# Optimization experiments

Measured on AMD Instinct MI355X. Metric: run time of the kernel, lower is better.

The kernel has to match this reference:

```python
import jax, jax.numpy as jnp
import numpy as np

BETA = 0.1
MARGIN = 0.1
LOSS_WEIGHT = 1.0
K = 4          # num_negative_samples_per_positive
EPS = 1e-6
C, D, P = 100000, 256, 65536


def _energy(p, c):
    """Euclidean entailment-cone energy: relu(apex_angle(p,c) - aperture(p))."""
    diff = c - p
    num = jnp.sum(c * c, -1) - jnp.sum(p * p, -1) - jnp.sum(diff * diff, -1)
    norm_p = jnp.linalg.norm(p, axis=-1)
    denom = 2.0 * norm_p * jnp.linalg.norm(diff, axis=-1) + EPS
    cosang = jnp.clip(num / denom, -1.0 + EPS, 1.0 - EPS)
    ang = jnp.arccos(cosang)
    aperture = jnp.arcsin(jnp.clip(BETA / (norm_p + EPS), 0.0, 1.0 - EPS))
    return jax.nn.relu(ang - aperture)


def setup_inputs() -> dict:
    key = jax.random.key(0)
    k1, k2, k3 = jax.random.split(key, 3)
    prototypes = jax.random.normal(k1, (C, D), dtype=jnp.float32)
    pairs = jax.random.randint(k2, (P, 2), 0, C, dtype=jnp.int32)
    neg_c = jax.random.randint(k3, (P * K,), 0, C, dtype=jnp.int32)
    return {"prototypes": prototypes, "pairs": pairs, "neg_c": neg_c}


def reference(prototypes, pairs, neg_c):
    # positive pairs: (parent, child) gathers
    p_pos = prototypes[pairs[:, 0]]                    # [P, D]
    c_pos = prototypes[pairs[:, 1]]                    # [P, D]
    avg_pos = _energy(p_pos, c_pos).mean()

    # negatives: each positive parent repeated K times vs sampled neg children
    neg_p_idx = jnp.repeat(pairs[:, 0], K)             # [P*K]
    p_neg = prototypes[neg_p_idx]                      # [P*K, D]
    c_neg = prototypes[neg_c]                          # [P*K, D]
    avg_neg = jax.nn.relu(MARGIN - _energy(p_neg, c_neg)).mean()

    return (avg_pos + avg_neg) * 0.5 * LOSS_WEIGHT
```

## Files before the change

kernel.cpp:

```cpp
#include <hip/hip_runtime.h>

#define BETA   0.1f
#define MARGIN 0.1f
#define EPSF   1e-6f
#define KNEG   4

__device__ __forceinline__ float gsum16(float v) {
    #pragma unroll
    for (int off = 8; off >= 1; off >>= 1) v += __shfl_xor(v, off, 64);
    return v;
}
__device__ __forceinline__ float gmax16(float v) {
    #pragma unroll
    for (int off = 8; off >= 1; off >>= 1) v = fmaxf(v, __shfl_xor(v, off, 64));
    return v;
}
__device__ __forceinline__ float wave_sum(float v) {
    #pragma unroll
    for (int off = 32; off >= 1; off >>= 1) v += __shfl_xor(v, off, 64);
    return v;
}
__device__ __forceinline__ float dot4(float4 a, float4 b) {
    return a.x*b.x + a.y*b.y + a.z*b.z + a.w*b.w;
}

__global__ __launch_bounds__(256) void cvt_i4(
    const float* __restrict__ in, uint2* __restrict__ tab,
    float4* __restrict__ side, int C)
{
    const int sl  = threadIdx.x & 15;
    const int row = (blockIdx.x * 256 + threadIdx.x) >> 4;
    if (row >= C) return;
    const float4* src = (const float4*)(in + (size_t)row * 256);
    float4 v0 = src[4*sl+0], v1 = src[4*sl+1], v2 = src[4*sl+2], v3 = src[4*sl+3];
    float f[16] = { v0.x, v0.y, v0.z, v0.w,  v1.x, v1.y, v1.z, v1.w,
                    v2.x, v2.y, v2.z, v2.w,  v3.x, v3.y, v3.z, v3.w };
    float am = 0.f;
    #pragma unroll
    for (int d = 0; d < 16; ++d) am = fmaxf(am, fabsf(f[d]));
    am = gmax16(am);
    const float inv = (am > 0.f) ? (7.5f / am) : 0.f;
    unsigned u0 = 0, u1 = 0;
    #pragma unroll
    for (int n = 0; n < 8; ++n) {
        int c = (int)rintf(f[n] * inv);
        c = (c < -8) ? -8 : ((c > 7) ? 7 : c);
        u0 |= (unsigned)(c + 8) << (4 * n);
    }
    #pragma unroll
    for (int n = 0; n < 8; ++n) {
        int c = (int)rintf(f[8 + n] * inv);
        c = (c < -8) ? -8 : ((c > 7) ? 7 : c);
        u1 |= (unsigned)(c + 8) << (4 * n);
    }
    tab[(size_t)row * 16 + sl] = make_uint2(u0, u1);
    float ss = gsum16(dot4(v0,v0) + dot4(v1,v1) + dot4(v2,v2) + dot4(v3,v3));
    if (sl == 0) {
        float np = sqrtf(ss);
        float ap = asinf(fminf(fmaxf(BETA / (np + EPSF), 0.f), 1.f - EPSF));
        side[row] = make_float4(ss, ap, am * (1.f / 7.5f), 0.f);
    }
}

__device__ __forceinline__ float codes_dot(uint2 cu, const float* pf) {
    float acc = 0.f;
    #pragma unroll
    for (int n = 0; n < 8; ++n)
        acc = fmaf((float)((cu.x >> (4*n)) & 0xF), pf[n], acc);
    #pragma unroll
    for (int n = 0; n < 8; ++n)
        acc = fmaf((float)((cu.y >> (4*n)) & 0xF), pf[8 + n], acc);
    return acc;
}

__global__ __launch_bounds__(256) void cone_main_i4(
    const uint2*  __restrict__ tab,
    const float4* __restrict__ side,
    const int*    __restrict__ pairs,
    const int*    __restrict__ negc,
    float*        __restrict__ part,
    int P)
{
    const int lane = threadIdx.x & 63;
    const int wid  = threadIdx.x >> 6;
    const int sub  = lane >> 4;
    const int sl   = lane & 15;
    const int pair = (blockIdx.x * 4 + wid) * 4 + sub;

    float pos_e = 0.f, neg_e = 0.f;
    if (pair < P) {
        const int pi = pairs[2 * pair];
        const int i0 = pairs[2 * pair + 1];
        const int i1 = negc[4 * pair + 0];
        const int i2 = negc[4 * pair + 1];
        const int i3 = negc[4 * pair + 2];
        const int i4 = negc[4 * pair + 3];

        uint2 pu  = tab[(size_t)pi * 16 + sl];
        uint2 cu0 = tab[(size_t)i0 * 16 + sl];
        uint2 cu1 = tab[(size_t)i1 * 16 + sl];
        uint2 cu2 = tab[(size_t)i2 * 16 + sl];
        uint2 cu3 = tab[(size_t)i3 * 16 + sl];
        uint2 cu4 = tab[(size_t)i4 * 16 + sl];

        int tidx = pi;
        tidx = (sl == 1) ? i0 : tidx;
        tidx = (sl == 2) ? i1 : tidx;
        tidx = (sl == 3) ? i2 : tidx;
        tidx = (sl == 4) ? i3 : tidx;
        tidx = (sl == 5) ? i4 : tidx;
        float4 sd = side[tidx];

        const int base = sub * 16;
        const float p2 = __shfl(sd.x, base + 0, 64);
        const float ap = __shfl(sd.y, base + 0, 64);
        const float sp = __shfl(sd.z, base + 0, 64);
        const float np = sqrtf(p2);

        float pf[16];
        #pragma unroll
        for (int n = 0; n < 8; ++n) pf[n]     = (float)((pu.x >> (4*n)) & 0xF) - 8.f;
        #pragma unroll
        for (int n = 0; n < 8; ++n) pf[8 + n] = (float)((pu.y >> (4*n)) & 0xF) - 8.f;
        float s = 0.f;
        #pragma unroll
        for (int d = 0; d < 16; ++d) s += pf[d];
        const float SP = gsum16(s);

#define CONE_STEP(J, CU)                                                      \
        {                                                                     \
            const float draw = gsum16(codes_dot(CU, pf)) - 8.f * SP;          \
            const float c2 = __shfl(sd.x, base + 1 + J, 64);                  \
            const float sc = __shfl(sd.z, base + 1 + J, 64);                  \
            const float dot = draw * sp * sc;                                 \
            const float num = 2.f * (dot - p2);                               \
            const float d2  = fmaxf(c2 + p2 - 2.f * dot, 0.f);                \
            const float den = 2.f * np * sqrtf(d2) + EPSF;                    \
            const float ca  = fminf(fmaxf(num / den, -1.f + EPSF), 1.f - EPSF);\
            const float e   = fmaxf(acosf(ca) - ap, 0.f);                     \
            if (J == 0) pos_e = e;                                            \
            else        neg_e += fmaxf(MARGIN - e, 0.f);                      \
        }
        CONE_STEP(0, cu0)
        CONE_STEP(1, cu1)
        CONE_STEP(2, cu2)
        CONE_STEP(3, cu3)
        CONE_STEP(4, cu4)
#undef CONE_STEP
    }

    __shared__ float spos[16], sneg[16];
    if (sl == 0) { spos[wid * 4 + sub] = pos_e; sneg[wid * 4 + sub] = neg_e; }
    __syncthreads();
    if (threadIdx.x == 0) {
        float ps = 0.f, ns = 0.f;
        #pragma unroll
        for (int i = 0; i < 16; ++i) { ps += spos[i]; ns += sneg[i]; }
        part[2 * blockIdx.x]     = ps;
        part[2 * blockIdx.x + 1] = ns;
    }
}

__global__ __launch_bounds__(256) void cone_main_f32(
    const float* __restrict__ proto,
    const int*   __restrict__ pairs,
    const int*   __restrict__ negc,
    float*       __restrict__ part,
    int P)
{
    const int lane = threadIdx.x & 63;
    const int wid  = threadIdx.x >> 6;
    const int sub  = lane >> 4;
    const int sl   = lane & 15;
    const int pair = (blockIdx.x * 4 + wid) * 4 + sub;

    float pos_e = 0.f, neg_e = 0.f;
    if (pair < P) {
        const int pi = pairs[2 * pair];
        const int i0 = pairs[2 * pair + 1];
        const int i1 = negc[4 * pair + 0];
        const int i2 = negc[4 * pair + 1];
        const int i3 = negc[4 * pair + 2];
        const int i4 = negc[4 * pair + 3];

        const float4* prow = (const float4*)(proto + (size_t)pi * 256);
        float4 pv[4];
        #pragma unroll
        for (int r = 0; r < 4; ++r) pv[r] = prow[sl + 16 * r];

        float pp = 0.f;
        #pragma unroll
        for (int r = 0; r < 4; ++r) pp += dot4(pv[r], pv[r]);
        float p2     = gsum16(pp);
        float norm_p = sqrtf(p2);
        float apert  = asinf(fminf(fmaxf(BETA / (norm_p + EPSF), 0.f), 1.f - EPSF));

#define CONE_F32_STEP(J, IDX)                                                 \
        {                                                                     \
            const float4* crow = (const float4*)(proto + (size_t)(IDX) * 256);\
            float cc = 0.f, dd = 0.f;                                         \
            _Pragma("unroll")                                                 \
            for (int r = 0; r < 4; ++r) {                                     \
                float4 c = crow[sl + 16 * r], p = pv[r];                      \
                cc += dot4(c, c);                                             \
                float dx = c.x-p.x, dy = c.y-p.y, dz = c.z-p.z, dw = c.w-p.w; \
                dd += dx*dx + dy*dy + dz*dz + dw*dw;                          \
            }                                                                 \
            float c2 = gsum16(cc);                                            \
            float d2 = gsum16(dd);                                            \
            float num    = c2 - p2 - d2;                                      \
            float den    = 2.f * norm_p * sqrtf(d2) + EPSF;                   \
            float cosang = fminf(fmaxf(num / den, -1.f + EPSF), 1.f - EPSF);  \
            float e      = fmaxf(acosf(cosang) - apert, 0.f);                 \
            if (J == 0) pos_e = e;                                            \
            else        neg_e += fmaxf(MARGIN - e, 0.f);                      \
        }
        CONE_F32_STEP(0, i0)
        CONE_F32_STEP(1, i1)
        CONE_F32_STEP(2, i2)
        CONE_F32_STEP(3, i3)
        CONE_F32_STEP(4, i4)
#undef CONE_F32_STEP
    }

    __shared__ float sp[16], sn[16];
    if (sl == 0) { sp[wid * 4 + sub] = pos_e; sn[wid * 4 + sub] = neg_e; }
    __syncthreads();
    if (threadIdx.x == 0) {
        float ps = 0.f, ns = 0.f;
        #pragma unroll
        for (int i = 0; i < 16; ++i) { ps += sp[i]; ns += sn[i]; }
        part[2 * blockIdx.x]     = ps;
        part[2 * blockIdx.x + 1] = ns;
    }
}

__global__ __launch_bounds__(1024) void cone_final(
    const float* __restrict__ part, float* __restrict__ out, int nblocks, int P)
{
    float ps = 0.f, ns = 0.f;
    for (int i = threadIdx.x; i < nblocks; i += 1024) {
        ps += part[2 * i];
        ns += part[2 * i + 1];
    }
    ps = wave_sum(ps);
    ns = wave_sum(ns);
    const int lane = threadIdx.x & 63, wid = threadIdx.x >> 6;
    __shared__ float sp[16], sn[16];
    if (lane == 0) { sp[wid] = ps; sn[wid] = ns; }
    __syncthreads();
    if (threadIdx.x == 0) {
        float tp = 0.f, tn = 0.f;
        #pragma unroll
        for (int i = 0; i < 16; ++i) { tp += sp[i]; tn += sn[i]; }
        float fP = (float)P;
        out[0] = (tp / fP + tn / (fP * (float)KNEG)) * 0.5f;
    }
}

extern "C" void kernel_launch(void* const* d_in, const int* in_sizes, int n_in,
                              void* d_out, int out_size, void* d_ws, size_t ws_size,
                              hipStream_t stream) {
    const float* proto = (const float*)d_in[0];
    const int*   pairs = (const int*)d_in[1];
    const int*   negc  = (const int*)d_in[2];
    const int P = in_sizes[1] / 2;
    const int C = in_sizes[0] / 256;
    const int nblocks = (P + 15) / 16;

    const size_t tab_bytes  = (size_t)C * 128;
    const size_t side_bytes = (size_t)C * 16;
    const size_t part_bytes = (size_t)nblocks * 2 * sizeof(float);
    const size_t need = tab_bytes + side_bytes + part_bytes;

    if (ws_size >= need) {
        char* base = (char*)d_ws;
        uint2*  tab  = (uint2*)base;
        float4* side = (float4*)(base + tab_bytes);
        float*  part = (float*)(base + tab_bytes + side_bytes);

        cvt_i4<<<(C + 15) / 16, 256, 0, stream>>>(proto, tab, side, C);
        cone_main_i4<<<nblocks, 256, 0, stream>>>(tab, side, pairs, negc, part, P);
        cone_final<<<1, 1024, 0, stream>>>(part, (float*)d_out, nblocks, P);
    } else {
        float* part = (float*)d_ws;
        cone_main_f32<<<nblocks, 256, 0, stream>>>(proto, pairs, negc, part, P);
        cone_final<<<1, 1024, 0, stream>>>(part, (float*)d_out, nblocks, P);
    }
}
```

Measured before the change: 172.3 us.

## Use signed int4 codes with sdot8 and spread acos across lanes

Quantization now stores signed 4-bit codes at scale 7 instead of offset codes at 7.5, so the per-row dot products can use the hardware sdot8 integer instruction with an integer group reduction. This replaces the float unpack-and-fma loop and the offset correction term. The five acos evaluations per pair are spread across lanes, each lane computing one, followed by a reduction. The coarser quantization scale slightly changes accuracy.

```diff
diff --git a/kernel.cpp b/kernel.cpp
--- a/kernel.cpp
+++ b/kernel.cpp
@@ -6,6 +6,11 @@
 #define KNEG   4
 
 __device__ __forceinline__ float gsum16(float v) {
+    #pragma unroll
+    for (int off = 8; off >= 1; off >>= 1) v += __shfl_xor(v, off, 64);
+    return v;
+}
+__device__ __forceinline__ int gsum16i(int v) {
     #pragma unroll
     for (int off = 8; off >= 1; off >>= 1) v += __shfl_xor(v, off, 64);
     return v;
@@ -39,38 +44,49 @@
     #pragma unroll
     for (int d = 0; d < 16; ++d) am = fmaxf(am, fabsf(f[d]));
     am = gmax16(am);
-    const float inv = (am > 0.f) ? (7.5f / am) : 0.f;
+    const float inv = (am > 0.f) ? (7.0f / am) : 0.f;
     unsigned u0 = 0, u1 = 0;
     #pragma unroll
     for (int n = 0; n < 8; ++n) {
         int c = (int)rintf(f[n] * inv);
         c = (c < -8) ? -8 : ((c > 7) ? 7 : c);
-        u0 |= (unsigned)(c + 8) << (4 * n);
+        u0 |= ((unsigned)c & 0xFu) << (4 * n);
     }
     #pragma unroll
     for (int n = 0; n < 8; ++n) {
         int c = (int)rintf(f[8 + n] * inv);
         c = (c < -8) ? -8 : ((c > 7) ? 7 : c);
-        u1 |= (unsigned)(c + 8) << (4 * n);
+        u1 |= ((unsigned)c & 0xFu) << (4 * n);
     }
     tab[(size_t)row * 16 + sl] = make_uint2(u0, u1);
     float ss = gsum16(dot4(v0,v0) + dot4(v1,v1) + dot4(v2,v2) + dot4(v3,v3));
     if (sl == 0) {
         float np = sqrtf(ss);
         float ap = asinf(fminf(fmaxf(BETA / (np + EPSF), 0.f), 1.f - EPSF));
-        side[row] = make_float4(ss, ap, am * (1.f / 7.5f), 0.f);
-    }
-}
-
-__device__ __forceinline__ float codes_dot(uint2 cu, const float* pf) {
-    float acc = 0.f;
-    #pragma unroll
-    for (int n = 0; n < 8; ++n)
-        acc = fmaf((float)((cu.x >> (4*n)) & 0xF), pf[n], acc);
-    #pragma unroll
-    for (int n = 0; n < 8; ++n)
-        acc = fmaf((float)((cu.y >> (4*n)) & 0xF), pf[8 + n], acc);
+        side[row] = make_float4(ss, ap, am * (1.f / 7.0f), 0.f);
+    }
+}
+
+__device__ __forceinline__ int nib_dot(uint2 a, uint2 b) {
+#if __has_builtin(__builtin_amdgcn_sdot8)
+    int d = __builtin_amdgcn_sdot8((int)a.x, (int)b.x, 0, false);
+    return  __builtin_amdgcn_sdot8((int)a.y, (int)b.y, d, false);
+#else
+    int acc = 0;
+    #pragma unroll
+    for (int n = 0; n < 8; ++n) {
+        int pa = ((int)(a.x << (28 - 4*n))) >> 28;
+        int pb = ((int)(b.x << (28 - 4*n))) >> 28;
+        acc += pa * pb;
+    }
+    #pragma unroll
+    for (int n = 0; n < 8; ++n) {
+        int pa = ((int)(a.y << (28 - 4*n))) >> 28;
+        int pb = ((int)(b.y << (28 - 4*n))) >> 28;
+        acc += pa * pb;
+    }
     return acc;
+#endif
 }
 
 __global__ __launch_bounds__(256) void cone_main_i4(
@@ -117,19 +133,11 @@
         const float sp = __shfl(sd.z, base + 0, 64);
         const float np = sqrtf(p2);
 
-        float pf[16];
-        #pragma unroll
-        for (int n = 0; n < 8; ++n) pf[n]     = (float)((pu.x >> (4*n)) & 0xF) - 8.f;
-        #pragma unroll
-        for (int n = 0; n < 8; ++n) pf[8 + n] = (float)((pu.y >> (4*n)) & 0xF) - 8.f;
-        float s = 0.f;
-        #pragma unroll
-        for (int d = 0; d < 16; ++d) s += pf[d];
-        const float SP = gsum16(s);
+        float my_ca = 1.f;
 
 #define CONE_STEP(J, CU)                                                      \
         {                                                                     \
-            const float draw = gsum16(codes_dot(CU, pf)) - 8.f * SP;          \
+            const float draw = (float)gsum16i(nib_dot(pu, CU));               \
             const float c2 = __shfl(sd.x, base + 1 + J, 64);                  \
             const float sc = __shfl(sd.z, base + 1 + J, 64);                  \
             const float dot = draw * sp * sc;                                 \
@@ -137,9 +145,7 @@
             const float d2  = fmaxf(c2 + p2 - 2.f * dot, 0.f);                \
             const float den = 2.f * np * sqrtf(d2) + EPSF;                    \
             const float ca  = fminf(fmaxf(num / den, -1.f + EPSF), 1.f - EPSF);\
-            const float e   = fmaxf(acosf(ca) - ap, 0.f);                     \
-            if (J == 0) pos_e = e;                                            \
-            else        neg_e += fmaxf(MARGIN - e, 0.f);                      \
+            my_ca = (sl == J) ? ca : my_ca;                                   \
         }
         CONE_STEP(0, cu0)
         CONE_STEP(1, cu1)
@@ -147,6 +153,12 @@
         CONE_STEP(3, cu3)
         CONE_STEP(4, cu4)
 #undef CONE_STEP
+
+        const float ang = acosf(my_ca);
+        const float e   = fmaxf(ang - ap, 0.f);
+        pos_e = (sl == 0) ? e : 0.f;
+        const float neg_c = (sl >= 1 && sl <= 4) ? fmaxf(MARGIN - e, 0.f) : 0.f;
+        neg_e = gsum16(neg_c);
     }
 
     __shared__ float spos[16], sneg[16];
```

After: 165.1 us. -4.2%, faster.
